# Optimization experiments

Hardware: AMD Instinct MI355X
Metric: run time of the kernel (lower is better)

The kernel has to match this reference:

```python
import jax, jax.numpy as jnp
import numpy as np
from jax import lax


def _ln(x, g, b, eps=1e-5):
    m = jnp.mean(x, axis=-1, keepdims=True)
    v = jnp.mean((x - m) ** 2, axis=-1, keepdims=True)
    return (x - m) / jnp.sqrt(v + eps) * g + b


def _lin(x, w, b):  # torch Linear: w [out,in]
    return x @ w.T + b


def _conv(x, w, b, stride, pad):
    y = lax.conv_general_dilated(x, w, (stride, stride), pad,
                                 dimension_numbers=('NCHW', 'OIHW', 'NCHW'))
    return y + b[None, :, None, None]


def _haar_dwt(x):
    # J=1 haar, zero mode, even H/W: per 2x2 block [[a,b],[c,d]]
    a = x[:, :, 0::2, 0::2]
    bb = x[:, :, 0::2, 1::2]
    c = x[:, :, 1::2, 0::2]
    d = x[:, :, 1::2, 1::2]
    ll = (a + bb + c + d) * 0.5
    lohi = (a - bb + c - d) * 0.5  # band 0 (col-high)
    hilo = (a + bb - c - d) * 0.5  # band 1 (row-high)
    hihi = (a - bb - c + d) * 0.5  # band 2
    return ll, lohi, hilo, hihi


def _cross_attention(q, k, v):
    # q,k,v: [b, d, c]; 8 equal chunks along d; softmax over QUERY axis (torch dim=1)
    b, d, c = q.shape
    chunk = d // 8
    qc = q.reshape(b, 8, chunk, c)
    kc = k.reshape(b, 8, chunk, c)
    vc = v.reshape(b, 8, chunk, c)
    att = jnp.einsum('bnqc,bnkc->bnqk', qc, kc) * (8.0 ** -0.5)
    att = jax.nn.softmax(att, axis=2)  # normalize over q (matches F.softmax dim=1)
    out = jnp.einsum('bnqk,bnkc->bnqc', att, vc)
    return out.reshape(b, d, c)


def _ffn(x, ln1_g, ln1_b, fc1_w, fc1_b, div_w, div_b, fc2_w, fc2_b,
         ln3_g, ln3_b, fc3a_w, fc3a_b, fc3b_w, fc3b_b, lnn_g, lnn_b, act_w, act_b):
    x1 = jax.nn.gelu(_lin(_ln(x, ln1_g, ln1_b), fc1_w, fc1_b), approximate=False)
    x2 = jax.nn.gelu(_lin(x, div_w, div_b), approximate=False) - x1
    x2 = jax.nn.gelu(_lin(x2, fc2_w, fc2_b), approximate=False)
    x3 = _lin(jax.nn.gelu(_lin(_ln(x, ln3_g, ln3_b), fc3a_w, fc3a_b), approximate=False), fc3b_w, fc3b_b)
    gate = jax.nn.sigmoid(_lin(x, act_w, act_b))
    # dropout(0.5) is identity in eval mode
    return gate * _ln(x2 + x3, lnn_g, lnn_b)


def _resize_bilinear_ac(x, oh, ow):
    # bilinear, align_corners=True
    B, C, H, W = x.shape
    def idx(n_in, n_out):
        pos = jnp.linspace(0.0, n_in - 1.0, n_out)
        i0 = jnp.floor(pos).astype(jnp.int32)
        i1 = jnp.minimum(i0 + 1, n_in - 1)
        return i0, i1, (pos - i0).astype(x.dtype)
    y0, y1, wy = idx(H, oh)
    x0, x1, wx = idx(W, ow)
    r = x[:, :, y0, :] * (1 - wy)[None, None, :, None] + x[:, :, y1, :] * wy[None, None, :, None]
    return r[:, :, :, x0] * (1 - wx)[None, None, None, :] + r[:, :, :, x1] * wx[None, None, None, :]


def setup_inputs() -> dict:
    key = jax.random.key(0)
    ks = jax.random.split(key, 25)
    B, Cin, H, W = 16, 128, 128, 128
    Ch = 128  # out_planes // 2
    def nrm(k, shp, s=0.02):
        return jax.random.normal(k, shp, jnp.float32) * s
    inp = {
        'x': jax.random.normal(ks[0], (B, Cin, H, W), jnp.float32),
        'conv1_w': nrm(ks[1], (Ch, 2 * Cin, 1, 1)), 'conv1_b': jnp.zeros((Ch,), jnp.float32),
        'l1_w': nrm(ks[2], (Ch, Cin, 4, 4)), 'l1_b': jnp.zeros((Ch,), jnp.float32),
        'ln1_g': jnp.ones((Ch,), jnp.float32), 'ln1_b': jnp.zeros((Ch,), jnp.float32),
        'fc1_w': nrm(ks[3], (Ch, Ch)), 'fc1_b': jnp.zeros((Ch,), jnp.float32),
        'div_w': nrm(ks[4], (Ch, Ch)), 'div_b': jnp.zeros((Ch,), jnp.float32),
        'fc2_w': nrm(ks[5], (Ch, Ch)), 'fc2_b': jnp.zeros((Ch,), jnp.float32),
        'ln3_g': jnp.ones((Ch,), jnp.float32), 'ln3_b': jnp.zeros((Ch,), jnp.float32),
        'fc3a_w': nrm(ks[6], (Ch, Ch)), 'fc3a_b': jnp.zeros((Ch,), jnp.float32),
        'fc3b_w': nrm(ks[7], (Ch, Ch)), 'fc3b_b': jnp.zeros((Ch,), jnp.float32),
        'lnn_g': jnp.ones((Ch,), jnp.float32), 'lnn_b': jnp.zeros((Ch,), jnp.float32),
        'act_w': nrm(ks[8], (Ch, Ch)), 'act_b': jnp.zeros((Ch,), jnp.float32),
    }
    return inp


def reference(x, conv1_w, conv1_b, l1_w, l1_b, ln1_g, ln1_b, fc1_w, fc1_b,
              div_w, div_b, fc2_w, fc2_b, ln3_g, ln3_b, fc3a_w, fc3a_b,
              fc3b_w, fc3b_b, lnn_g, lnn_b, act_w, act_b):
    dw = jax.nn.relu(_conv(x, l1_w, l1_b, 2, ((1, 1), (1, 1))))
    yL, y_HL, y_LH, y_HH = _haar_dwt(x)
    y = _conv(jnp.concatenate((y_HL, y_LH), axis=1), conv1_w, conv1_b, 1, ((0, 0), (0, 0)))
    b, c, h, w = y.shape
    y_t = y.transpose(0, 2, 3, 1).reshape(b, h * w, c)
    yL_t = yL.transpose(0, 2, 3, 1).reshape(b, h * w, c)
    yHH_t = y_HH.transpose(0, 2, 3, 1).reshape(b, h * w, c)
    att = _cross_attention(yL_t, y_t, yHH_t)
    att = _ffn(att, ln1_g, ln1_b, fc1_w, fc1_b, div_w, div_b, fc2_w, fc2_b,
               ln3_g, ln3_b, fc3a_w, fc3a_b, fc3b_w, fc3b_b, lnn_g, lnn_b, act_w, act_b)
    att = att.reshape(b, h, w, c).transpose(0, 3, 1, 2)
    y_img = y_t.reshape(b, h, w, c).transpose(0, 3, 1, 2)
    down_2x = _resize_bilinear_ac(x, h, w)
    att = att * (down_2x - dw)
    return att + y_img
```

## Files before the change

kernel.cpp:

```cpp
#include <hip/hip_runtime.h>
#include <cmath>


#define EPI_NONE 0
#define EPI_GELU 1
#define EPI_GELU_SUB 2
#define EPI_ADD 3
#define EPI_SIGMOID 4
#define EPI_EXP 5

typedef unsigned short u16;
typedef __bf16 v8bf __attribute__((ext_vector_type(8)));
typedef float f32x4 __attribute__((ext_vector_type(4)));

__device__ __forceinline__ float gelu_f(float v) {
  return 0.5f * v * (1.f + erff(v * 0.70710678118654752f));
}
__device__ __forceinline__ float sigmoid_f(float v) {
  return 1.f / (1.f + __expf(-v));
}
__device__ __forceinline__ float bf2f(u16 h) {
  return __uint_as_float((unsigned)h << 16);
}
__device__ __forceinline__ u16 f2bf(float f) {
  unsigned u = __float_as_uint(f);
  return (u16)((u + 0x7fffu + ((u >> 16) & 1u)) >> 16);
}
__device__ __forceinline__ unsigned f2bf_pk(float lo, float hi) {
  unsigned a = __float_as_uint(lo), b = __float_as_uint(hi);
  a = (a + 0x7fffu + ((a >> 16) & 1u)) >> 16;
  b = (b + 0x7fffu + ((b >> 16) & 1u)) >> 16;
  return a | (b << 16);
}
__device__ __forceinline__ void gld_lds16(const void* g, void* l) {
  __builtin_amdgcn_global_load_lds(
      (const __attribute__((address_space(1))) unsigned int*)g,
      (__attribute__((address_space(3))) unsigned int*)l, 16, 0, 0);
}

__global__ __launch_bounds__(256) void pre_k(const float* __restrict__ x,
                                             u16* __restrict__ yL16,
                                             u16* __restrict__ yHHt16,
                                             u16* __restrict__ hllh16,
                                             u16* __restrict__ xpt) {
  int gx = blockIdx.x;
  int jt = gx & 1, cit = gx >> 1;
  int i = blockIdx.y, b = blockIdx.z;
  int j0 = jt * 32, ci0 = cit * 32;
  int tx = threadIdx.x & 31, ty = threadIdx.x >> 5;
  __shared__ float sll[32][33], shl[32][33], slh[32][33], shh[32][33];
  if (gx == 0) {
    int pl = 1 + ((threadIdx.x >> 7) << 1);
    long off = ((long)(b * 4 + pl) * 4160 + (long)i * 65) * 128 + (threadIdx.x & 127);
    xpt[off] = 0;
  } else if (gx == 1) {
    int pl = (threadIdx.x >> 7) << 1;
    long off = ((long)(b * 4 + pl) * 4160 + (long)i * 65 + 64) * 128 + (threadIdx.x & 127);
    xpt[off] = 0;
  }
  const float2* x2 = (const float2*)x;
#pragma unroll
  for (int k = 0; k < 4; ++k) {
    int ci = ty + 8 * k;
    long base = (((long)b * 128 + ci0 + ci) * 128 + 2 * i) * 64 + j0 + tx;
    float2 ab = x2[base];
    float2 cd = x2[base + 64];
    float a = ab.x, bb = ab.y, c = cd.x, d = cd.y;
    sll[ci][tx] = (a + bb + c + d) * 0.5f;
    shl[ci][tx] = (a - bb + c - d) * 0.5f;
    slh[ci][tx] = (a + bb - c - d) * 0.5f;
    shh[ci][tx] = (a - bb - c + d) * 0.5f;
  }
  __syncthreads();
  long tok = (long)b * 4096 + i * 64 + j0;
#pragma unroll
  for (int k = 0; k < 4; ++k) {
    int row = ty + 8 * k;
    long t = tok + row;
    float ll = sll[tx][row], hl = shl[tx][row], lh = slh[tx][row],
          hh = shh[tx][row];
    yL16[t * 128 + ci0 + tx] = f2bf(ll);
    hllh16[t * 256 + ci0 + tx] = f2bf(hl);
    hllh16[t * 256 + 128 + ci0 + tx] = f2bf(lh);
    yHHt16[(long)(ci0 + row) * 65536 + tok + tx] = f2bf(shh[row][tx]);
    float pa = 0.5f * (ll + hl + lh + hh);
    float pv = 0.5f * (ll - hl + lh - hh);
    float pc = 0.5f * (ll + hl - lh - hh);
    float pd = 0.5f * (ll - hl - lh + hh);
    int ci = j0 + row, c = ci0 + tx;
    long rb = (long)(b * 4) * 4160 + (long)i * 65;
    xpt[(rb + ci) * 128 + c] = f2bf(pa);
    xpt[(rb + 4160 + ci + 1) * 128 + c] = f2bf(pv);
    xpt[(rb + 8320 + ci) * 128 + c] = f2bf(pc);
    xpt[(rb + 12480 + ci + 1) * 128 + c] = f2bf(pd);
  }
}

__global__ __launch_bounds__(256) void wcvt8_k(
    const float* __restrict__ a0, const float* __restrict__ a1,
    const float* __restrict__ a2, const float* __restrict__ a3,
    const float* __restrict__ a4, const float* __restrict__ a5,
    const float* __restrict__ a6, const float* __restrict__ a7,
    unsigned* __restrict__ dst, unsigned* __restrict__ zp) {
  if (blockIdx.x >= 768) {
    zp[(blockIdx.x - 768) * 256 + threadIdx.x] = 0;
    return;
  }
  int f = blockIdx.x * 256 + threadIdx.x;
  int e = 2 * f;
  if (e < 262144) {
    int ch = e >> 13, kg = (e >> 10) & 7, n = (e >> 3) & 127, ke = e & 7;
    int k = ch * 64 + kg * 8 + ke;
    int stg = ch >> 2, sub = ch & 3;
    int kwsel = sub >> 1, chalf = sub & 1;
    int kh = stg >> 1, cp = stg & 1;
    int kw = cp ? (kwsel ? 2 : 0) : (kwsel ? 3 : 1);
    int c = chalf * 64 + (k & 63);
    long si = (((long)n * 128 + c) * 4 + kh) * 4 + kw;
    dst[f] = f2bf_pk(a0[si], a0[si + 16]);
    return;
  }
  const float* s; int b;
  if (e < 294912)      { s = a1; b = 262144; }
  else if (e < 311296) { s = a2; b = 294912; }
  else if (e < 327680) { s = a3; b = 311296; }
  else if (e < 344064) { s = a4; b = 327680; }
  else if (e < 360448) { s = a5; b = 344064; }
  else if (e < 376832) { s = a6; b = 360448; }
  else                 { s = a7; b = 376832; }
  dst[f] = f2bf_pk(s[e - b], s[e - b + 1]);
}

template <int AMODE, int EPI>
__global__ __launch_bounds__(256) void gemm16_k(
    const u16* __restrict__ A, long sA, int lda,
    const u16* __restrict__ B, long sB, int ldb,
    u16* __restrict__ C, long sC, int ldc,
    int K, float alpha, const float* __restrict__ bias,
    const u16* __restrict__ aux, const float* __restrict__ sc) {
  __shared__ __align__(16) char smem[32768];
  char* As = smem;
  char* Bs = smem + 16384;
  int z = blockIdx.z;
  int tid = threadIdx.x, lane = tid & 63, w = tid >> 6;
  int wm = w >> 1, wn = w & 1, l15 = lane & 15, l4 = lane >> 4;
  const u16* Ab = A + (long)z * sA + (long)blockIdx.x * 128 * lda;
  const u16* Bb = B + (long)z * sB + (long)blockIdx.y * 128 * ldb;
  const float* scz = (AMODE == 1) ? sc + (long)z * K : nullptr;
  int sm = tid >> 3, skg = tid & 7;
  int sbase = sm * 128 + ((skg ^ (sm & 7)) << 4);
  uint4 pa[4], pb[4];

  auto loadAB = [&](int k0) {
#pragma unroll
    for (int u = 0; u < 4; ++u) {
      pb[u] = *(const uint4*)(Bb + (long)(sm + 32 * u) * ldb + k0 + skg * 8);
      uint4 v = *(const uint4*)(Ab + (long)(sm + 32 * u) * lda + k0 + skg * 8);
      if (AMODE == 1) {
        float4 s0 = *(const float4*)(scz + k0 + skg * 8);
        float4 s1 = *(const float4*)(scz + k0 + skg * 8 + 4);
        v.x = f2bf_pk(bf2f((u16)(v.x & 0xffff)) * s0.x, bf2f((u16)(v.x >> 16)) * s0.y);
        v.y = f2bf_pk(bf2f((u16)(v.y & 0xffff)) * s0.z, bf2f((u16)(v.y >> 16)) * s0.w);
        v.z = f2bf_pk(bf2f((u16)(v.z & 0xffff)) * s1.x, bf2f((u16)(v.z >> 16)) * s1.y);
        v.w = f2bf_pk(bf2f((u16)(v.w & 0xffff)) * s1.z, bf2f((u16)(v.w >> 16)) * s1.w);
      }
      pa[u] = v;
    }
  };

  f32x4 acc[4][4] = {};
  loadAB(0);
  int nch = K >> 6;
  for (int ch = 0; ch < nch; ++ch) {
    __syncthreads();
#pragma unroll
    for (int u = 0; u < 4; ++u) {
      *(uint4*)(As + sbase + u * 4096) = pa[u];
      *(uint4*)(Bs + sbase + u * 4096) = pb[u];
    }
    __syncthreads();
    if (ch + 1 < nch) loadAB((ch + 1) << 6);
#pragma unroll
    for (int s = 0; s < 2; ++s) {
      int ko = (((s << 2) | l4) ^ (l15 & 7)) << 4;
      v8bf af[4], bfr[4];
#pragma unroll
      for (int t = 0; t < 4; ++t) {
        af[t] = *(const v8bf*)(As + (64 * wm + 16 * t + l15) * 128 + ko);
        bfr[t] = *(const v8bf*)(Bs + (64 * wn + 16 * t + l15) * 128 + ko);
      }
#pragma unroll
      for (int mt = 0; mt < 4; ++mt)
#pragma unroll
        for (int nt = 0; nt < 4; ++nt)
          acc[mt][nt] = __builtin_amdgcn_mfma_f32_16x16x32_bf16(af[mt], bfr[nt], acc[mt][nt], 0, 0, 0);
    }
  }
  u16* Cb = C + (long)z * sC;
#pragma unroll
  for (int mt = 0; mt < 4; ++mt) {
#pragma unroll
    for (int nt = 0; nt < 4; ++nt) {
      f32x4 a = acc[mt][nt];
      int n = blockIdx.y * 128 + 64 * wn + 16 * nt + l15;
      float bv = bias ? bias[n] : 0.f;
#pragma unroll
      for (int r = 0; r < 4; ++r) {
        long m = (long)blockIdx.x * 128 + 64 * wm + 16 * mt + 4 * l4 + r;
        float v = a[r] * alpha + bv;
        if (EPI == EPI_GELU) v = gelu_f(v);
        else if (EPI == EPI_GELU_SUB) v = gelu_f(v) - bf2f(aux[m * ldc + n]);
        else if (EPI == EPI_ADD) v += bf2f(aux[m * ldc + n]);
        else if (EPI == EPI_SIGMOID) v = sigmoid_f(v);
        else if (EPI == EPI_EXP) v = __expf(v);
        Cb[m * ldc + n] = f2bf(v);
      }
    }
  }
}

__global__ __launch_bounds__(256) __attribute__((amdgpu_waves_per_eu(4)))
void conv4g_k(const u16* __restrict__ xpt, const u16* __restrict__ wb,
              const float* __restrict__ bias, const u16* __restrict__ zp,
              u16* __restrict__ dw16) {
  __shared__ __align__(16) char smem[33280];
  char* As = smem;
  int raw = blockIdx.x;
  int swz = (raw & 7) * 128 + (raw >> 3);
  int oi = swz & 63, b = swz >> 6;
  int tid = threadIdx.x, lane = tid & 63, w = tid >> 6;
  int wm = w >> 1, wn = w & 1, l15 = lane & 15, l4 = lane >> 4;
  f32x4 acc[2][4] = {};

  auto issueA = [&](int stg2, int bsel) {
    int kh = stg2 >> 1, cp2 = stg2 & 1;
    int roff = (kh == 0) ? -1 : (kh == 3) ? 1 : 0;
    int ri = oi + roff;
    int ph = (((kh + 1) & 1) << 1) | cp2;
    const u16* rowb = ((unsigned)ri < 64u)
        ? xpt + ((long)(b * 4 + ph) * 4160 + (long)ri * 65) * 128
        : zp;
    char* lb = As + bsel * 16640 + w * 1024;
#pragma unroll
    for (int i = 0; i < 4; ++i) {
      int d = i * 4096 + w * 1024 + lane * 16;
      int slot = d >> 8, cg = (d >> 4) & 15;
      gld_lds16(rowb + slot * 128 + ((cg ^ ((slot - cp2) & 7)) << 3),
                lb + i * 4096);
    }
    if (tid < 16) {
      gld_lds16(rowb + 64 * 128 + ((lane ^ ((64 - cp2) & 7)) << 3),
                As + bsel * 16640 + 16384);
    }
  };

  issueA(0, 0);
  for (int stg = 0; stg < 8; ++stg) {
    __syncthreads();
    if (stg < 7) issueA(stg + 1, (stg + 1) & 1);
    const char* Ab = As + (stg & 1) * 16640;
    int cp2 = stg & 1;
#pragma unroll
    for (int sub = 0; sub < 4; ++sub) {
      int chunk = stg * 4 + sub;
      const int kwsel = sub >> 1, chalf = sub & 1;
#pragma unroll
      for (int s = 0; s < 2; ++s) {
        v8bf bw[4], af[2];
#pragma unroll
        for (int nt = 0; nt < 4; ++nt) {
          int row = 64 * wn + 16 * nt + l15;
          bw[nt] = *(const v8bf*)(wb + ((long)(chunk * 8 + s * 4 + l4) * 128 + row) * 8);
        }
#pragma unroll
        for (int mt = 0; mt < 2; ++mt) {
          int slot = 32 * wm + 16 * mt + l15 + kwsel;
          int cg = chalf * 8 + s * 4 + l4;
          af[mt] = *(const v8bf*)(Ab + slot * 256 + ((cg ^ ((slot - cp2) & 7)) << 4));
        }
#pragma unroll
        for (int mt = 0; mt < 2; ++mt)
#pragma unroll
          for (int nt = 0; nt < 4; ++nt)
            acc[mt][nt] = __builtin_amdgcn_mfma_f32_16x16x32_bf16(
                af[mt], bw[nt], acc[mt][nt], 0, 0, 0);
      }
    }
  }
  __syncthreads();
  float* buf = (float*)(smem + w * 2176);
  long obase = ((long)b * 128) * 4096 + oi * 64;
#pragma unroll
  for (int cg = 0; cg < 4; ++cg) {
    int co = 64 * wn + 16 * cg + l15;
    float bv = bias[co];
#pragma unroll
    for (int mt = 0; mt < 2; ++mt) {
      f32x4 a = acc[mt][cg];
#pragma unroll
      for (int r = 0; r < 4; ++r)
        buf[l15 * 34 + 16 * mt + 4 * l4 + r] = fmaxf(a[r] + bv, 0.f);
    }
    __syncthreads();
#pragma unroll
    for (int it = 0; it < 8; ++it) {
      int row = it * 2 + (lane >> 5);
      int mcol = lane & 31;
      int coz = 64 * wn + 16 * cg + row;
      dw16[obase + (long)coz * 4096 + 32 * wm + mcol] = f2bf(buf[row * 34 + mcol]);
    }
    __syncthreads();
  }
}

__global__ __launch_bounds__(256) void ssum_k(const u16* __restrict__ E,
                                              float* __restrict__ sc) {
  int z = blockIdx.y;
  int k = blockIdx.x * 256 + threadIdx.x;
  const u16* Eb = E + (long)z * 262144 + k;
  float s = 0.f;
#pragma unroll 8
  for (int q = 0; q < 512; ++q) s += bf2f(Eb[(long)q * 512]);
  sc[(long)z * 512 + k] = 1.f / s;
}

__global__ __launch_bounds__(256) void ln16_k(const u16* __restrict__ X,
                                              const float* __restrict__ g,
                                              const float* __restrict__ bt,
                                              const u16* __restrict__ gate,
                                              u16* __restrict__ Y) {
  int t = (blockIdx.x * 256 + threadIdx.x) >> 6;
  int lane = threadIdx.x & 63;
  const u16* xr = X + (long)t * 128;
  float v0 = bf2f(xr[lane]), v1 = bf2f(xr[lane + 64]);
  float s = v0 + v1, sq = v0 * v0 + v1 * v1;
#pragma unroll
  for (int off = 32; off > 0; off >>= 1) {
    s += __shfl_xor(s, off);
    sq += __shfl_xor(sq, off);
  }
  float mean = s * 0.0078125f;
  float var = sq * 0.0078125f - mean * mean;
  float rstd = rsqrtf(var + 1e-5f);
  float y0 = (v0 - mean) * rstd * g[lane] + bt[lane];
  float y1 = (v1 - mean) * rstd * g[lane + 64] + bt[lane + 64];
  if (gate) {
    y0 *= bf2f(gate[(long)t * 128 + lane]);
    y1 *= bf2f(gate[(long)t * 128 + lane + 64]);
  }
  Y[(long)t * 128 + lane] = f2bf(y0);
  Y[(long)t * 128 + lane + 64] = f2bf(y1);
}

__global__ __launch_bounds__(256) void combine_k(const u16* __restrict__ attf,
                                                 const u16* __restrict__ yt,
                                                 const u16* __restrict__ dw16,
                                                 const float* __restrict__ x,
                                                 float* __restrict__ out) {
  int gx = blockIdx.x;
  int jt = gx & 1, cot = gx >> 1;
  int i = blockIdx.y, b = blockIdx.z;
  int j0 = jt * 32, co0 = cot * 32;
  int tx = threadIdx.x & 31, ty = threadIdx.x >> 5;
  __shared__ float sa[32][33], sy[32][33];
  long tokbase = (long)b * 4096 + i * 64 + j0;
#pragma unroll
  for (int k = 0; k < 4; ++k) {
    int row = ty + 8 * k;
    long idx = (tokbase + row) * 128 + co0 + tx;
    sa[row][tx] = bf2f(attf[idx]);
    sy[row][tx] = bf2f(yt[idx]);
  }
  __syncthreads();
  float py = (float)(i * 127) / 63.0f;
  int y0 = (int)py;
  int y1 = min(y0 + 1, 127);
  float wy = py - (float)y0;
  int j = j0 + tx;
  float px = (float)(j * 127) / 63.0f;
  int x0 = (int)px;
  int x1 = min(x0 + 1, 127);
  float wx = px - (float)x0;
#pragma unroll
  for (int k = 0; k < 4; ++k) {
    int co = co0 + ty + 8 * k;
    const float* xb = x + (((long)b * 128 + co) * 128) * 128;
    float r0 = xb[y0 * 128 + x0] * (1.f - wx) + xb[y0 * 128 + x1] * wx;
    float r1 = xb[y1 * 128 + x0] * (1.f - wx) + xb[y1 * 128 + x1] * wx;
    float d2 = r0 * (1.f - wy) + r1 * wy;
    long oidx = (((long)b * 128 + co) * 64 + i) * 64 + j;
    float dwv = bf2f(dw16[oidx]);
    out[oidx] = sa[tx][ty + 8 * k] * (d2 - dwv) + sy[tx][ty + 8 * k];
  }
}

extern "C" void kernel_launch(void* const* d_in, const int* in_sizes, int n_in,
                              void* d_out, int out_size, void* d_ws, size_t ws_size,
                              hipStream_t stream) {
  const float* x = (const float*)d_in[0];
  const float* w1 = (const float*)d_in[1];
  const float* b1 = (const float*)d_in[2];
  const float* l1w = (const float*)d_in[3];
  const float* l1b = (const float*)d_in[4];
  const float* ln1g = (const float*)d_in[5];
  const float* ln1b = (const float*)d_in[6];
  const float* fc1w = (const float*)d_in[7];
  const float* fc1b = (const float*)d_in[8];
  const float* divw = (const float*)d_in[9];
  const float* divb = (const float*)d_in[10];
  const float* fc2w = (const float*)d_in[11];
  const float* fc2b = (const float*)d_in[12];
  const float* ln3g = (const float*)d_in[13];
  const float* ln3b = (const float*)d_in[14];
  const float* fc3aw = (const float*)d_in[15];
  const float* fc3ab = (const float*)d_in[16];
  const float* fc3bw = (const float*)d_in[17];
  const float* fc3bb = (const float*)d_in[18];
  const float* lnng = (const float*)d_in[19];
  const float* lnnb = (const float*)d_in[20];
  const float* actw = (const float*)d_in[21];
  const float* actb = (const float*)d_in[22];

  char* W = (char*)d_ws;
  u16* yL16 = (u16*)(W);
  u16* hllh16 = (u16*)(W + 16777216L);
  u16* yHHt16 = (u16*)(W + 50331648L);
  u16* y16 = (u16*)(W + 67108864L);
  u16* S16 = (u16*)(W + 83886080L);
  u16* attO16 = (u16*)(W + 150994944L);
  u16* dw16 = (u16*)(W + 167772160L);
  u16* t1 = (u16*)(W + 184549376L);
  u16* t2 = (u16*)(W + 201326592L);
  u16* t3 = (u16*)(W + 218103808L);
  u16* t4 = (u16*)(W + 234881024L);
  float* sc = (float*)(W + 251658240L);
  u16* wall = (u16*)(W + 251920384L);
  u16* l1wb = wall;
  u16* w1b = wall + 262144;
  u16* fc1b16 = wall + 294912;
  u16* divb16 = wall + 311296;
  u16* fc2b16 = wall + 327680;
  u16* fc3ab16 = wall + 344064;
  u16* fc3bb16 = wall + 360448;
  u16* actb16 = wall + 376832;
  u16* xpt16 = S16;
  u16* zp16 = (u16*)(W + 152043520L);

  dim3 blk(256);
  const float qk_scale = 0.35355339059327373f;

  wcvt8_k<<<dim3(785), blk, 0, stream>>>(l1w, w1, fc1w, divw, fc2w, fc3aw,
                                         fc3bw, actw, (unsigned*)wall,
                                         (unsigned*)zp16);
  pre_k<<<dim3(8, 64, 16), blk, 0, stream>>>(x, yL16, yHHt16, hllh16, xpt16);
  gemm16_k<0, EPI_NONE><<<dim3(512, 1, 1), blk, 0, stream>>>(
      hllh16, 0, 256, w1b, 0, 256, y16, 0, 128, 256, 1.f, b1, nullptr, nullptr);
  conv4g_k<<<dim3(1024), blk, 0, stream>>>(xpt16, l1wb, l1b, zp16, dw16);
  gemm16_k<0, EPI_EXP><<<dim3(4, 4, 128), blk, 0, stream>>>(
      yL16, 65536, 128, y16, 65536, 128, S16, 262144, 512, 128, qk_scale,
      nullptr, nullptr, nullptr);
  ssum_k<<<dim3(2, 128), blk, 0, stream>>>(S16, sc);
  gemm16_k<1, EPI_NONE><<<dim3(4, 1, 128), blk, 0, stream>>>(
      S16, 262144, 512, yHHt16, 512, 65536, attO16, 65536, 128, 512, 1.f,
      nullptr, nullptr, sc);
  ln16_k<<<16384, blk, 0, stream>>>(attO16, ln1g, ln1b, nullptr, t1);
  gemm16_k<0, EPI_GELU><<<dim3(512, 1, 1), blk, 0, stream>>>(
      t1, 0, 128, fc1b16, 0, 128, t2, 0, 128, 128, 1.f, fc1b, nullptr, nullptr);
  gemm16_k<0, EPI_GELU_SUB><<<dim3(512, 1, 1), blk, 0, stream>>>(
      attO16, 0, 128, divb16, 0, 128, t3, 0, 128, 128, 1.f, divb, t2, nullptr);
  gemm16_k<0, EPI_GELU><<<dim3(512, 1, 1), blk, 0, stream>>>(
      t3, 0, 128, fc2b16, 0, 128, t4, 0, 128, 128, 1.f, fc2b, nullptr, nullptr);
  ln16_k<<<16384, blk, 0, stream>>>(attO16, ln3g, ln3b, nullptr, t1);
  gemm16_k<0, EPI_GELU><<<dim3(512, 1, 1), blk, 0, stream>>>(
      t1, 0, 128, fc3ab16, 0, 128, t3, 0, 128, 128, 1.f, fc3ab, nullptr, nullptr);
  gemm16_k<0, EPI_ADD><<<dim3(512, 1, 1), blk, 0, stream>>>(
      t3, 0, 128, fc3bb16, 0, 128, t1, 0, 128, 128, 1.f, fc3bb, t4, nullptr);
  gemm16_k<0, EPI_SIGMOID><<<dim3(512, 1, 1), blk, 0, stream>>>(
      attO16, 0, 128, actb16, 0, 128, t3, 0, 128, 128, 1.f, actb, nullptr, nullptr);
  ln16_k<<<16384, blk, 0, stream>>>(t1, lnng, lnnb, t3, t2);
  combine_k<<<dim3(8, 64, 16), blk, 0, stream>>>(t2, y16, dw16, x, (float*)d_out);
}
```

Baseline: 665.1 us.

## Restructure Haar preprocessing kernel for vectorized packed bf16 stores

The preprocessing kernel now gives each block a full row of 128 channels and loops over four 16-column tiles. It stores only partial sums and differences in shared memory, and rebuilds the Haar bands and the pixel-shuffled conv input algebraically from them. Outputs are written as 16-byte packed bf16 vectors instead of scalar 2-byte stores, which should cut store transaction count. The trade-off is a grid eight times smaller with a serial loop and extra barriers per block, which lowers parallelism.

```diff
diff --git a/kernel.cpp b/kernel.cpp
--- a/kernel.cpp
+++ b/kernel.cpp
@@ -38,61 +38,73 @@
       (__attribute__((address_space(3))) unsigned int*)l, 16, 0, 0);
 }
 
-__global__ __launch_bounds__(256) void pre_k(const float* __restrict__ x,
-                                             u16* __restrict__ yL16,
-                                             u16* __restrict__ yHHt16,
-                                             u16* __restrict__ hllh16,
-                                             u16* __restrict__ xpt) {
-  int gx = blockIdx.x;
-  int jt = gx & 1, cit = gx >> 1;
-  int i = blockIdx.y, b = blockIdx.z;
-  int j0 = jt * 32, ci0 = cit * 32;
-  int tx = threadIdx.x & 31, ty = threadIdx.x >> 5;
-  __shared__ float sll[32][33], shl[32][33], slh[32][33], shh[32][33];
-  if (gx == 0) {
-    int pl = 1 + ((threadIdx.x >> 7) << 1);
-    long off = ((long)(b * 4 + pl) * 4160 + (long)i * 65) * 128 + (threadIdx.x & 127);
-    xpt[off] = 0;
-  } else if (gx == 1) {
-    int pl = (threadIdx.x >> 7) << 1;
-    long off = ((long)(b * 4 + pl) * 4160 + (long)i * 65 + 64) * 128 + (threadIdx.x & 127);
-    xpt[off] = 0;
-  }
+#define PKST(dst, X, Y, OP)                                                    \
+  *(uint4*)(dst) = uint4{                                                      \
+      f2bf_pk((X[0] OP Y[0]) * 0.5f, (X[1] OP Y[1]) * 0.5f),                   \
+      f2bf_pk((X[2] OP Y[2]) * 0.5f, (X[3] OP Y[3]) * 0.5f),                   \
+      f2bf_pk((X[4] OP Y[4]) * 0.5f, (X[5] OP Y[5]) * 0.5f),                   \
+      f2bf_pk((X[6] OP Y[6]) * 0.5f, (X[7] OP Y[7]) * 0.5f)};
+
+__global__ __launch_bounds__(256) __attribute__((amdgpu_waves_per_eu(4)))
+void pre_k(const float* __restrict__ x, u16* __restrict__ yL16,
+           u16* __restrict__ yHHt16, u16* __restrict__ hllh16,
+           u16* __restrict__ xpt) {
+  int i = blockIdx.x, b = blockIdx.y;
+  int tid = threadIdx.x;
+  __shared__ float su[16][133], sv[16][133], ss[16][133], st[16][133];
   const float2* x2 = (const float2*)x;
-#pragma unroll
-  for (int k = 0; k < 4; ++k) {
-    int ci = ty + 8 * k;
-    long base = (((long)b * 128 + ci0 + ci) * 128 + 2 * i) * 64 + j0 + tx;
-    float2 ab = x2[base];
-    float2 cd = x2[base + 64];
-    float a = ab.x, bb = ab.y, c = cd.x, d = cd.y;
-    sll[ci][tx] = (a + bb + c + d) * 0.5f;
-    shl[ci][tx] = (a - bb + c - d) * 0.5f;
-    slh[ci][tx] = (a + bb - c - d) * 0.5f;
-    shh[ci][tx] = (a - bb - c + d) * 0.5f;
-  }
-  __syncthreads();
-  long tok = (long)b * 4096 + i * 64 + j0;
-#pragma unroll
-  for (int k = 0; k < 4; ++k) {
-    int row = ty + 8 * k;
-    long t = tok + row;
-    float ll = sll[tx][row], hl = shl[tx][row], lh = slh[tx][row],
-          hh = shh[tx][row];
-    yL16[t * 128 + ci0 + tx] = f2bf(ll);
-    hllh16[t * 256 + ci0 + tx] = f2bf(hl);
-    hllh16[t * 256 + 128 + ci0 + tx] = f2bf(lh);
-    yHHt16[(long)(ci0 + row) * 65536 + tok + tx] = f2bf(shh[row][tx]);
-    float pa = 0.5f * (ll + hl + lh + hh);
-    float pv = 0.5f * (ll - hl + lh - hh);
-    float pc = 0.5f * (ll + hl - lh - hh);
-    float pd = 0.5f * (ll - hl - lh + hh);
-    int ci = j0 + row, c = ci0 + tx;
-    long rb = (long)(b * 4) * 4160 + (long)i * 65;
-    xpt[(rb + ci) * 128 + c] = f2bf(pa);
-    xpt[(rb + 4160 + ci + 1) * 128 + c] = f2bf(pv);
-    xpt[(rb + 8320 + ci) * 128 + c] = f2bf(pc);
-    xpt[(rb + 12480 + ci + 1) * 128 + c] = f2bf(pd);
+  long tokb = (long)b * 4096 + (long)i * 64;
+  long prow = (long)(b * 4) * 4160 + (long)i * 65;
+  if (tid < 64) {
+    int ph = tid >> 4, l16 = tid & 15;
+    int hc = (ph & 1) ? 0 : 64;
+    *(uint4*)(xpt + (prow + (long)ph * 4160 + hc) * 128 + l16 * 8) =
+        uint4{0u, 0u, 0u, 0u};
+  }
+  int txl = tid & 15, tyl = tid >> 4;
+  int r2 = tid >> 4, c8 = (tid & 15) * 8;
+  int ct = tid >> 1, th = (tid & 1) * 8;
+  for (int jt = 0; jt < 4; ++jt) {
+    int j0 = jt * 16;
+    if (jt) __syncthreads();
+#pragma unroll
+    for (int k = 0; k < 8; ++k) {
+      int ch = tyl + 16 * k;
+      long base = (((long)(b * 128 + ch) * 128) + 2 * i) * 64 + j0 + txl;
+      float2 ab = x2[base];
+      float2 cd = x2[base + 64];
+      su[txl][ch] = ab.x + ab.y;
+      sv[txl][ch] = ab.x - ab.y;
+      ss[txl][ch] = cd.x + cd.y;
+      st[txl][ch] = cd.x - cd.y;
+    }
+    __syncthreads();
+    float u[8], v[8], s[8], t[8];
+#pragma unroll
+    for (int e = 0; e < 8; ++e) {
+      u[e] = su[r2][c8 + e];
+      v[e] = sv[r2][c8 + e];
+      s[e] = ss[r2][c8 + e];
+      t[e] = st[r2][c8 + e];
+    }
+    long tg = tokb + j0 + r2;
+    int ci = j0 + r2;
+    PKST(yL16 + tg * 128 + c8, u, s, +)
+    PKST(hllh16 + tg * 256 + c8, v, t, +)
+    PKST(hllh16 + tg * 256 + 128 + c8, u, s, -)
+    PKST(xpt + (prow + ci) * 128 + c8, u, v, +)
+    PKST(xpt + (prow + 4160 + ci + 1) * 128 + c8, u, v, -)
+    PKST(xpt + (prow + 8320 + ci) * 128 + c8, s, t, +)
+    PKST(xpt + (prow + 12480 + ci + 1) * 128 + c8, s, t, -)
+    unsigned hw[4];
+#pragma unroll
+    for (int q = 0; q < 4; ++q) {
+      float h0 = (sv[th + 2 * q][ct] - st[th + 2 * q][ct]) * 0.5f;
+      float h1 = (sv[th + 2 * q + 1][ct] - st[th + 2 * q + 1][ct]) * 0.5f;
+      hw[q] = f2bf_pk(h0, h1);
+    }
+    *(uint4*)(yHHt16 + (long)ct * 65536 + tokb + j0 + th) =
+        uint4{hw[0], hw[1], hw[2], hw[3]};
   }
 }
 
@@ -452,7 +464,7 @@
   wcvt8_k<<<dim3(785), blk, 0, stream>>>(l1w, w1, fc1w, divw, fc2w, fc3aw,
                                          fc3bw, actw, (unsigned*)wall,
                                          (unsigned*)zp16);
-  pre_k<<<dim3(8, 64, 16), blk, 0, stream>>>(x, yL16, yHHt16, hllh16, xpt16);
+  pre_k<<<dim3(64, 16), blk, 0, stream>>>(x, yL16, yHHt16, hllh16, xpt16);
   gemm16_k<0, EPI_NONE><<<dim3(512, 1, 1), blk, 0, stream>>>(
       hllh16, 0, 256, w1b, 0, 256, y16, 0, 128, 256, 1.f, b1, nullptr, nullptr);
   conv4g_k<<<dim3(1024), blk, 0, stream>>>(xpt16, l1wb, l1b, zp16, dw16);
```

Result: no change. 670.9 us (+0.9%).
